# Optimization experiments

Measured on AMD Instinct MI355X. Metric: run time of the kernel, lower is better.

Reference implementation:

```python
import jax, jax.numpy as jnp
import numpy as np

ALPHA = 0.5
SPLIT_RATIO = 0.5
NUM_HEADS = 12
LN_EPS = 1e-6


def _layernorm(x, g, b):
    m = x.mean(-1, keepdims=True)
    v = ((x - m) ** 2).mean(-1, keepdims=True)
    return (x - m) * jax.lax.rsqrt(v + LN_EPS) * g + b


def setup_inputs() -> dict:
    key = jax.random.key(0)
    ks = jax.random.split(key, 8)
    B, N1, C, L, Hm = 16, 197, 768, 4, 3072
    s = 0.02
    return {
        "x": jax.random.normal(ks[0], (B, N1, C), jnp.float32),
        "glb_cls_attn": jax.random.uniform(ks[1], (B, N1 - 1), jnp.float32),
        "split_w": jax.random.normal(ks[2], (C, 4 * C), jnp.float32) * s,
        "split_b": jnp.zeros((4 * C,), jnp.float32),
        "ln1_g": jnp.ones((L, C), jnp.float32),
        "ln1_b": jnp.zeros((L, C), jnp.float32),
        "qkv_w": jax.random.normal(ks[3], (L, C, 3 * C), jnp.float32) * s,
        "qkv_b": jnp.zeros((L, 3 * C), jnp.float32),
        "proj_w": jax.random.normal(ks[4], (L, C, C), jnp.float32) * s,
        "proj_b": jnp.zeros((L, C), jnp.float32),
        "ln2_g": jnp.ones((L, C), jnp.float32),
        "ln2_b": jnp.zeros((L, C), jnp.float32),
        "fc1_w": jax.random.normal(ks[5], (L, C, Hm), jnp.float32) * s,
        "fc1_b": jnp.zeros((L, Hm), jnp.float32),
        "fc2_w": jax.random.normal(ks[6], (L, Hm, C), jnp.float32) * s,
        "fc2_b": jnp.zeros((L, C), jnp.float32),
    }


def reference(x, glb_cls_attn, split_w, split_b, ln1_g, ln1_b, qkv_w, qkv_b,
              proj_w, proj_b, ln2_g, ln2_b, fc1_w, fc1_b, fc2_w, fc2_b):
    B, _, C = x.shape
    H = NUM_HEADS
    D = C // H
    scale = D ** -0.5

    # --- token split based on global cls attention importance ---
    cls_tok, tokens = x[:, :1], x[:, 1:]
    order = jnp.argsort(-glb_cls_attn, axis=1)  # descending importance
    tokens = jnp.take_along_axis(tokens, order[:, :, None], axis=1)
    n = tokens.shape[1]
    split_n = int(n * SPLIT_RATIO)
    st = tokens[:, :split_n] @ split_w + split_b          # [B, split_n, 4C]
    st = st.reshape(B, split_n * 4, C)                    # each token -> 4 tokens
    x = jnp.concatenate([cls_tok, st, tokens[:, split_n:]], axis=1)
    N = x.shape[1]
    glb = jnp.zeros((B, N - 1), x.dtype)

    def block(carry, p):
        x, g = carry
        g1, b1, qw, qb, pw, pb, g2, b2, w1, bb1, w2, bb2 = p
        h = _layernorm(x, g1, b1)
        qkv = (h @ qw + qb).reshape(B, N, 3, H, D).transpose(2, 0, 3, 1, 4)
        q, k, v = qkv[0], qkv[1], qkv[2]                  # [B,H,N,D]
        attn = jax.nn.softmax(jnp.einsum('bhnd,bhmd->bhnm', q, k) * scale, axis=-1)
        cls_attn = attn[:, :, 0, 1:].mean(axis=1)         # mean over heads, row 0
        o = jnp.einsum('bhnm,bhmd->bhnd', attn, v).transpose(0, 2, 1, 3).reshape(B, N, C)
        x = x + o @ pw + pb
        h2 = _layernorm(x, g2, b2)
        x = x + jax.nn.gelu(h2 @ w1 + bb1, approximate=False) @ w2 + bb2
        g = ALPHA * g + (1.0 - ALPHA) * cls_attn
        return (x, g), None

    (x, glb), _ = jax.lax.scan(
        block, (x, glb),
        (ln1_g, ln1_b, qkv_w, qkv_b, proj_w, proj_b,
         ln2_g, ln2_b, fc1_w, fc1_b, fc2_w, fc2_b))
    return x, glb
```

## Files before the change

### kernel.cpp

```cpp
#include <hip/hip_runtime.h>
#include <math.h>

typedef unsigned short u16;
typedef short s16x8 __attribute__((ext_vector_type(8)));
typedef float f32x4 __attribute__((ext_vector_type(4)));

#define BB 16
#define N1 197
#define NTOK 196
#define SPLITN 98
#define NN 491
#define CC 768
#define H3 2304
#define HM 3072
#define NH 12
#define NL 4
#define BN (BB*NN)
#define MSPLIT (BB*SPLITN)

__device__ __forceinline__ float b2f(u16 u) {
    union { unsigned int i; float f; } x; x.i = ((unsigned int)u) << 16; return x.f;
}
__device__ __forceinline__ u16 f2b(float f) {
    union { float f; unsigned int i; } x; x.f = f;
    unsigned int i = x.i;
    return (u16)((i + 0x7fffu + ((i >> 16) & 1u)) >> 16);
}
__device__ __forceinline__ float ldx(const void* p, long long i, int isf32) {
    return isf32 ? ((const float*)p)[i] : b2f(((const u16*)p)[i]);
}

__device__ __forceinline__ void gload_lds16(const u16* g, u16* l) {
    __builtin_amdgcn_global_load_lds(
        (const __attribute__((address_space(1))) unsigned int*)g,
        (__attribute__((address_space(3))) unsigned int*)l,
        16, 0, 0);
}

__global__ void detect_k(const void* __restrict__ ln1_g, int* __restrict__ flag) {
    unsigned int w = ((const unsigned int*)ln1_g)[0];
    *flag = (w == 0x3F800000u) ? 1 : 0;
}

__global__ void zero_out_k(u16* __restrict__ out, long long n) {
    long long idx = (long long)blockIdx.x * 256 + threadIdx.x;
    if (idx < n) out[idx] = 0;
}

__global__ void zero_glb_k(float* __restrict__ glb) {
    int idx = blockIdx.x * 256 + threadIdx.x;
    if (idx < BB * (NN - 1)) glb[idx] = 0.0f;
}

__global__ void sort_k(const void* __restrict__ g, int* __restrict__ order,
                       const int* __restrict__ dflag) {
    __shared__ float v[256];
    int isf32 = *dflag;
    int b = blockIdx.x, t = threadIdx.x;
    float vv = -1e30f;
    if (t < NTOK) {
        vv = ldx(g, (long long)b * NTOK + t, isf32);
        if (!(vv == vv)) vv = -1e30f;
    }
    v[t] = vv;
    __syncthreads();
    if (t < NTOK) {
        float mv = v[t]; int r = 0;
        for (int j = 0; j < NTOK; j++) {
            float vj = v[j];
            if (vj > mv || (vj == mv && j < t)) r++;
        }
        order[b * NTOK + r] = t;
    }
}

__device__ __forceinline__ int clamp_tok(int tok) {
    return (tok < 0) ? 0 : (tok > NTOK - 1 ? NTOK - 1 : tok);
}

__global__ void gather_split_k(const void* __restrict__ x_in, const int* __restrict__ order,
                               u16* __restrict__ Asp, const int* __restrict__ dflag) {
    int isf32 = *dflag;
    long long idx = (long long)blockIdx.x * 256 + threadIdx.x;
    if (idx >= (long long)MSPLIT * CC) return;
    int c = (int)(idx % CC); int m = (int)(idx / CC); int b = m / SPLITN, r = m % SPLITN;
    int tok = clamp_tok(order[b * NTOK + r]);
    Asp[idx] = f2b(ldx(x_in, ((long long)b * N1 + 1 + tok) * CC + c, isf32));
}

__global__ void build_x_k(const void* __restrict__ x_in, const u16* __restrict__ st,
                          const int* __restrict__ order, float* __restrict__ x,
                          const int* __restrict__ dflag) {
    int isf32 = *dflag;
    long long idx = (long long)blockIdx.x * 256 + threadIdx.x;
    if (idx >= (long long)BN * CC) return;
    int c = (int)(idx % CC);
    int m = (int)(idx / CC);
    int b = m / NN, pos = m % NN;
    float v;
    if (pos == 0) {
        v = ldx(x_in, (long long)b * N1 * CC + c, isf32);
    } else if (pos < 1 + 4 * SPLITN) {
        int tt = pos - 1; int r = tt >> 2, kq = tt & 3;
        v = b2f(st[((long long)b * SPLITN + r) * HM + kq * CC + c]);
    } else {
        int j = pos - (1 + 4 * SPLITN);
        int tok = clamp_tok(order[b * NTOK + SPLITN + j]);
        v = ldx(x_in, ((long long)b * N1 + 1 + tok) * CC + c, isf32);
    }
    x[idx] = v;
}

__global__ void transpose_off_k(const void* __restrict__ in, u16* __restrict__ out, int K, int N,
                                long long off, const int* __restrict__ dflag) {
    __shared__ u16 tile[32][33];
    int isf32 = *dflag;
    int n0 = blockIdx.x * 32, k0 = blockIdx.y * 32;
    int tx = threadIdx.x, ty = threadIdx.y;
    for (int i = ty; i < 32; i += 8)
        tile[i][tx] = f2b(ldx(in, off + (long long)(k0 + i) * N + n0 + tx, isf32));
    __syncthreads();
    for (int i = ty; i < 32; i += 8) out[(long long)(n0 + i) * K + k0 + tx] = tile[tx][i];
}

__global__ __launch_bounds__(256) void ln_k(const float* __restrict__ x, const void* __restrict__ g,
                                            const void* __restrict__ bgain, u16* __restrict__ h,
                                            int goff, const int* __restrict__ dflag) {
    __shared__ float sb[8];
    int isf32 = *dflag;
    int row = blockIdx.x, t = threadIdx.x;
    const float* xr = x + (long long)row * CC;
    float v0 = xr[t], v1 = xr[t + 256], v2 = xr[t + 512];
    float s = v0 + v1 + v2;
    for (int o = 32; o > 0; o >>= 1) s += __shfl_down(s, o, 64);
    int lane = t & 63, w = t >> 6;
    if (lane == 0) sb[w] = s;
    __syncthreads();
    float mean = (sb[0] + sb[1] + sb[2] + sb[3]) * (1.0f / 768.0f);
    float d0 = v0 - mean, d1 = v1 - mean, d2 = v2 - mean;
    float q = d0 * d0 + d1 * d1 + d2 * d2;
    for (int o = 32; o > 0; o >>= 1) q += __shfl_down(q, o, 64);
    if (lane == 0) sb[4 + w] = q;
    __syncthreads();
    float var = (sb[4] + sb[5] + sb[6] + sb[7]) * (1.0f / 768.0f);
    float rs = rsqrtf(var + 1e-6f);
    long long o0 = (long long)row * CC;
    h[o0 + t]       = f2b(d0 * rs * ldx(g, goff + t, isf32)       + ldx(bgain, goff + t, isf32));
    h[o0 + t + 256] = f2b(d1 * rs * ldx(g, goff + t + 256, isf32) + ldx(bgain, goff + t + 256, isf32));
    h[o0 + t + 512] = f2b(d2 * rs * ldx(g, goff + t + 512, isf32) + ldx(bgain, goff + t + 512, isf32));
}

template<int TBM, int TBN>
__global__ __launch_bounds__(256) void gemm_t(const u16* __restrict__ A, const u16* __restrict__ BT,
                                              const void* __restrict__ bias, int boff,
                                              void* __restrict__ out,
                                              int M, int N, int K, int mode,
                                              const int* __restrict__ dflag) {
    constexpr int WM = TBM / 2, WN = TBN / 2, FM = WM / 16, FN = WN / 16;
    constexpr int AI = TBM / 64;
    constexpr int BI = TBN / 64;
    __shared__ __align__(16) u16 As[2][TBM * 32];
    __shared__ __align__(16) u16 Bs[2][TBN * 32];
    int isf32 = *dflag;

    int gx = gridDim.x, gy = gridDim.y;
    int nwg = gx * gy;
    int bid0 = blockIdx.y * gx + blockIdx.x;
    int q = nwg >> 3, rr = nwg & 7;
    int xcd = bid0 & 7, sl = bid0 >> 3;
    int wg = (xcd < rr ? xcd * (q + 1) : rr * (q + 1) + (xcd - rr) * q) + sl;
    int by = wg % gy, bx = wg / gy;
    int m0 = bx * TBM, n0 = by * TBN;

    int t = threadIdx.x, wave = t >> 6, lane = t & 63;
    int wm = (wave >> 1) * WM, wn = (wave & 1) * WN;
    int fr = lane & 15, quad = lane >> 4;

    int srow = lane >> 2;
    int scol = ((lane & 3) ^ ((srow >> 1) & 3)) * 8;

    f32x4 acc[FM][FN];
#pragma unroll
    for (int i = 0; i < FM; i++)
#pragma unroll
        for (int j = 0; j < FN; j++) acc[i][j] = (f32x4){0.f, 0.f, 0.f, 0.f};

    const int nk = K >> 5;

    auto stage = [&](int buf, int k0) {
#pragma unroll
        for (int i = 0; i < AI; i++) {
            int r0 = wave * (TBM / 4) + i * 16;
            int row = m0 + r0 + srow;
            if (row > M - 1) row = M - 1;
            gload_lds16(&A[(long long)row * K + k0 + scol], &As[buf][r0 * 32]);
        }
#pragma unroll
        for (int i = 0; i < BI; i++) {
            int r0 = wave * (TBN / 4) + i * 16;
            gload_lds16(&BT[(long long)(n0 + r0 + srow) * K + k0 + scol], &Bs[buf][r0 * 32]);
        }
    };

    stage(0, 0);
    __syncthreads();
    int rofs = ((quad ^ ((fr >> 1) & 3)) * 8);
    for (int kt = 0; kt < nk; kt++) {
        int cur = kt & 1;
        if (kt + 1 < nk) stage(cur ^ 1, (kt + 1) << 5);
        s16x8 af[FM], bf2[FN];
#pragma unroll
        for (int i = 0; i < FM; i++)
            af[i] = *(const s16x8*)&As[cur][(wm + i * 16 + fr) * 32 + rofs];
#pragma unroll
        for (int j = 0; j < FN; j++)
            bf2[j] = *(const s16x8*)&Bs[cur][(wn + j * 16 + fr) * 32 + rofs];
#pragma unroll
        for (int i = 0; i < FM; i++)
#pragma unroll
            for (int j = 0; j < FN; j++)
                acc[i][j] = __builtin_amdgcn_mfma_f32_16x16x32_bf16(af[i], bf2[j], acc[i][j], 0, 0, 0);
        __syncthreads();
    }

#pragma unroll
    for (int i = 0; i < FM; i++) {
#pragma unroll
        for (int j = 0; j < FN; j++) {
#pragma unroll
            for (int r = 0; r < 4; r++) {
                int row = m0 + wm + i * 16 + quad * 4 + r;
                int col = n0 + wn + j * 16 + fr;
                if (row < M) {
                    float v = acc[i][j][r] + ldx(bias, boff + col, isf32);
                    long long idx = (long long)row * N + col;
                    if (mode == 1) ((u16*)out)[idx] = f2b(v);
                    else if (mode == 2) {
                        float gl = 0.5f * v * (1.0f + erff(v * 0.70710678118654752f));
                        ((u16*)out)[idx] = f2b(gl);
                    } else ((float*)out)[idx] += v;
                }
            }
        }
    }
}

__global__ __launch_bounds__(256, 2) void attn_mfma_k(const u16* __restrict__ qkv,
                                                      u16* __restrict__ o,
                                                      float* __restrict__ cls_partial, int b0) {
    int bh = blockIdx.y; int lb = bh / NH, h = bh % NH;
    int i0 = blockIdx.x * 64;
    int w = threadIdx.x >> 6, lane = threadIdx.x & 63;
    int fr = lane & 15, quad = lane >> 4;
    int fk = quad * 8;

    __shared__ __align__(16) u16 Qs[64][72];
    __shared__ __align__(16) u16 Ks[64][72];
    __shared__ __align__(16) u16 Vt[64][40];
    __shared__ __align__(16) u16 Pst[4][16][40];

    const long long rowbase = (long long)lb * NN * H3 + (long long)h * 64;

    {
        int t = threadIdx.x;
#pragma unroll
        for (int i = 0; i < 2; i++) {
            int e = t + i * 256;
            int r = e >> 3, c8 = (e & 7) * 8;
            uint4 v = make_uint4(0u, 0u, 0u, 0u);
            int qrow = i0 + r;
            if (qrow < NN) v = *(const uint4*)&qkv[rowbase + (long long)qrow * H3 + c8];
            *(uint4*)&Qs[r][c8] = v;
        }
    }
    __syncthreads();
    s16x8 aq0 = *(const s16x8*)&Qs[w * 16 + fr][fk];
    s16x8 aq1 = *(const s16x8*)&Qs[w * 16 + fr][32 + fk];

    f32x4 S[32];
#pragma unroll
    for (int i = 0; i < 32; i++) S[i] = (f32x4){0.f, 0.f, 0.f, 0.f};

#pragma unroll
    for (int kt = 0; kt < 8; kt++) {
        int tb = kt * 64;
        __syncthreads();
        {
            int t = threadIdx.x;
#pragma unroll
            for (int i = 0; i < 2; i++) {
                int e = t + i * 256;
                int r = e >> 3, c8 = (e & 7) * 8;
                uint4 v = make_uint4(0u, 0u, 0u, 0u);
                int krow = tb + r;
                if (krow < NN) v = *(const uint4*)&qkv[rowbase + (long long)krow * H3 + CC + c8];
                *(uint4*)&Ks[r][c8] = v;
            }
        }
        __syncthreads();
#pragma unroll
        for (int ct = 0; ct < 4; ct++) {
            s16x8 bk0 = *(const s16x8*)&Ks[ct * 16 + fr][fk];
            s16x8 bk1 = *(const s16x8*)&Ks[ct * 16 + fr][32 + fk];
            S[kt * 4 + ct] = __builtin_amdgcn_mfma_f32_16x16x32_bf16(aq0, bk0, S[kt * 4 + ct], 0, 0, 0);
            S[kt * 4 + ct] = __builtin_amdgcn_mfma_f32_16x16x32_bf16(aq1, bk1, S[kt * 4 + ct], 0, 0, 0);
        }
    }

    float mrow[4] = {-1e30f, -1e30f, -1e30f, -1e30f};
#pragma unroll
    for (int tl = 0; tl < 32; tl++) {
        int col = tl * 16 + fr;
        bool valid = col < NN;
#pragma unroll
        for (int r = 0; r < 4; r++) {
            float s = S[tl][r] * 0.125f;
            s = valid ? s : -1e30f;
            S[tl][r] = s;
            mrow[r] = fmaxf(mrow[r], s);
        }
    }
#pragma unroll
    for (int m = 1; m < 16; m <<= 1)
#pragma unroll
        for (int r = 0; r < 4; r++) mrow[r] = fmaxf(mrow[r], __shfl_xor(mrow[r], m, 64));
    float lrow[4] = {0.f, 0.f, 0.f, 0.f};
#pragma unroll
    for (int tl = 0; tl < 32; tl++)
#pragma unroll
        for (int r = 0; r < 4; r++) {
            float e = __expf(S[tl][r] - mrow[r]);
            S[tl][r] = e;
            lrow[r] += e;
        }
#pragma unroll
    for (int m = 1; m < 16; m <<= 1)
#pragma unroll
        for (int r = 0; r < 4; r++) lrow[r] += __shfl_xor(lrow[r], m, 64);
    float linv[4];
#pragma unroll
    for (int r = 0; r < 4; r++) linv[r] = 1.0f / lrow[r];

    if (blockIdx.x == 0 && w == 0 && quad == 0) {
        long long cbase = (long long)((b0 + lb) * NH + h) * (NN - 1);
        float inv = linv[0];
#pragma unroll
        for (int tl = 0; tl < 32; tl++) {
            int col = tl * 16 + fr;
            if (col >= 1 && col < NN) cls_partial[cbase + col - 1] = S[tl][0] * inv;
        }
    }

    f32x4 O[4];
#pragma unroll
    for (int d = 0; d < 4; d++) O[d] = (f32x4){0.f, 0.f, 0.f, 0.f};
#pragma unroll
    for (int kt2 = 0; kt2 < 16; kt2++) {
        int vb = kt2 * 32;
        __syncthreads();
        {
            int t = threadIdx.x;
            int r = t >> 3, c8 = (t & 7) * 8;
            uint4 v = make_uint4(0u, 0u, 0u, 0u);
            int vrow = vb + r;
            if (vrow < NN) v = *(const uint4*)&qkv[rowbase + (long long)vrow * H3 + 2 * CC + c8];
            union { uint4 u; u16 e[8]; } tmp; tmp.u = v;
#pragma unroll
            for (int j = 0; j < 8; j++) Vt[c8 + j][r] = tmp.e[j];
        }
#pragma unroll
        for (int tt = 0; tt < 2; tt++) {
            int tl = kt2 * 2 + tt;
#pragma unroll
            for (int r = 0; r < 4; r++)
                Pst[w][quad * 4 + r][tt * 16 + fr] = f2b(S[tl][r]);
        }
        __syncthreads();
        s16x8 ap = *(const s16x8*)&Pst[w][fr][fk];
#pragma unroll
        for (int dt = 0; dt < 4; dt++) {
            s16x8 bv = *(const s16x8*)&Vt[dt * 16 + fr][fk];
            O[dt] = __builtin_amdgcn_mfma_f32_16x16x32_bf16(ap, bv, O[dt], 0, 0, 0);
        }
    }

#pragma unroll
    for (int r = 0; r < 4; r++) {
        int qrow = i0 + w * 16 + quad * 4 + r;
        if (qrow < NN) {
            long long obase = ((long long)(b0 + lb) * NN + qrow) * CC + h * 64;
#pragma unroll
            for (int dt = 0; dt < 4; dt++)
                o[obase + dt * 16 + fr] = f2b(O[dt][r] * linv[r]);
        }
    }
}

__global__ void glb_update_k(const float* __restrict__ cls_partial, float* __restrict__ glb) {
    int idx = blockIdx.x * 256 + threadIdx.x;
    if (idx >= BB * (NN - 1)) return;
    int b = idx / (NN - 1), j = idx % (NN - 1);
    float s = 0;
    for (int h = 0; h < NH; h++) s += cls_partial[(long long)(b * NH + h) * (NN - 1) + j];
    glb[idx] = 0.5f * glb[idx] + 0.5f * (s / NH);
}

__global__ void finalize_k(const float* __restrict__ x, const float* __restrict__ glb,
                           void* __restrict__ out, const int* __restrict__ dflag) {
    int isf32 = *dflag;
    long long nx = (long long)BN * CC;
    long long nt = nx + (long long)BB * (NN - 1);
    long long idx = (long long)blockIdx.x * 256 + threadIdx.x;
    if (idx >= nt) return;
    float v = (idx < nx) ? x[idx] : glb[idx - nx];
    if (isf32) ((float*)out)[idx] = v;
    else ((u16*)out)[idx] = f2b(v);
}

static inline char* carve(char*& p, size_t bytes) {
    char* r = p;
    p += (bytes + 255) & ~(size_t)255;
    return r;
}
static inline size_t padb(size_t b) { return (b + 255) & ~(size_t)255; }

extern "C" void kernel_launch(void* const* d_in, const int* in_sizes, int n_in,
                              void* d_out, int out_size, void* d_ws, size_t ws_size,
                              hipStream_t stream) {
    const void* x_in    = d_in[0];
    const void* glb_in  = d_in[1];
    const void* split_w = d_in[2];
    const void* split_b = d_in[3];
    const void* ln1_g   = d_in[4];
    const void* ln1_b   = d_in[5];
    const void* qkv_w   = d_in[6];
    const void* qkv_b   = d_in[7];
    const void* proj_w  = d_in[8];
    const void* proj_b  = d_in[9];
    const void* ln2_g   = d_in[10];
    const void* ln2_b   = d_in[11];
    const void* fc1_w   = d_in[12];
    const void* fc1_b   = d_in[13];
    const void* fc2_w   = d_in[14];
    const void* fc2_b   = d_in[15];

    const size_t sz_x    = (size_t)BN * CC * 4;
    const size_t sz_h    = (size_t)BN * CC * 2;
    const size_t sz_wt   = (size_t)HM * CC * 2;
    const size_t sz_cls  = (size_t)BB * NH * (NN - 1) * 4;
    const size_t sz_glb  = (size_t)BB * (NN - 1) * 4;
    const size_t sz_ord  = (size_t)BB * NTOK * 4;

    const size_t rA = (size_t)BN * H3 * 2;
    const size_t rB = (size_t)(BN / 4) * HM * 2;
    const size_t rC = (size_t)MSPLIT * HM * 2;

    const size_t base = padb(sz_x) + padb(sz_h) + 2 * padb(sz_wt) + padb(sz_cls) +
                        padb(sz_glb) + padb(sz_ord) + 256;
    int tier; size_t rsz;
    if (ws_size >= base + padb(rA))      { tier = 0; rsz = rA; }
    else if (ws_size >= base + padb(rB)) { tier = 1; rsz = rB; }
    else if (ws_size >= base + padb(rC)) { tier = 2; rsz = rC; }
    else {
        zero_out_k<<<(int)(((long long)out_size + 255) / 256), 256, 0, stream>>>((u16*)d_out, (long long)out_size);
        return;
    }

    char* p = (char*)d_ws;
    float* x_f32   = (float*)carve(p, sz_x);
    u16* h_buf     = (u16*)carve(p, sz_h);
    u16* region1   = (u16*)carve(p, rsz);
    u16* wtA       = (u16*)carve(p, sz_wt);
    u16* wtB       = (u16*)carve(p, sz_wt);
    float* cls_par = (float*)carve(p, sz_cls);
    float* glb_f32 = (float*)carve(p, sz_glb);
    int* order     = (int*)carve(p, sz_ord);
    int* dflag     = (int*)carve(p, 256);
    u16* Asp       = wtB;

    auto gemm = [&](const u16* A, const u16* BT, const void* bias, int boff, void* out,
                    int M, int N, int K, int mode) {
        long long b128 = (long long)((M + 127) / 128) * (N / 128);
        if ((N & 127) == 0 && b128 >= 512)
            gemm_t<128, 128><<<dim3((M + 127) / 128, N / 128), 256, 0, stream>>>(
                A, BT, bias, boff, out, M, N, K, mode, dflag);
        else
            gemm_t<64, 64><<<dim3((M + 63) / 64, N / 64), 256, 0, stream>>>(
                A, BT, bias, boff, out, M, N, K, mode, dflag);
    };

    dim3 tb(32, 8);
    detect_k<<<1, 1, 0, stream>>>(ln1_g, dflag);
    zero_glb_k<<<(BB * (NN - 1) + 255) / 256, 256, 0, stream>>>(glb_f32);
    sort_k<<<BB, 256, 0, stream>>>(glb_in, order, dflag);
    gather_split_k<<<(MSPLIT * CC + 255) / 256, 256, 0, stream>>>(x_in, order, Asp, dflag);
    transpose_off_k<<<dim3(HM / 32, CC / 32), tb, 0, stream>>>(split_w, wtA, CC, HM, 0, dflag);
    gemm(Asp, wtA, split_b, 0, region1, MSPLIT, HM, CC, 1);
    build_x_k<<<(int)(((long long)BN * CC + 255) / 256), 256, 0, stream>>>(x_in, region1, order,
                                                                           x_f32, dflag);

    const int QTILES = (NN + 63) / 64;
    const int bch  = (tier == 0) ? BB : 4;
    const int nbch = BB / bch;
    const int matt = bch * NN;
    const int nmch = (tier == 0) ? 2 : (tier == 1) ? 4 : 8;
    const int mch  = BN / nmch;

    for (int l = 0; l < NL; l++) {
        transpose_off_k<<<dim3(H3 / 32, CC / 32), tb, 0, stream>>>(qkv_w, wtA, CC, H3,
                                                                   (long long)l * CC * H3, dflag);
        ln_k<<<BN, 256, 0, stream>>>(x_f32, ln1_g, ln1_b, h_buf, l * CC, dflag);
        for (int bc = 0; bc < nbch; bc++) {
            const u16* Ain = h_buf + (long long)bc * matt * CC;
            gemm(Ain, wtA, qkv_b, l * H3, region1, matt, H3, CC, 1);
            attn_mfma_k<<<dim3(QTILES, bch * NH), 256, 0, stream>>>(region1, h_buf, cls_par, bc * bch);
        }
        glb_update_k<<<(BB * (NN - 1) + 255) / 256, 256, 0, stream>>>(cls_par, glb_f32);
        transpose_off_k<<<dim3(CC / 32, CC / 32), tb, 0, stream>>>(proj_w, wtA, CC, CC,
                                                                   (long long)l * CC * CC, dflag);
        gemm(h_buf, wtA, proj_b, l * CC, x_f32, BN, CC, CC, 3);
        ln_k<<<BN, 256, 0, stream>>>(x_f32, ln2_g, ln2_b, h_buf, l * CC, dflag);
        transpose_off_k<<<dim3(HM / 32, CC / 32), tb, 0, stream>>>(fc1_w, wtA, CC, HM,
                                                                   (long long)l * CC * HM, dflag);
        transpose_off_k<<<dim3(CC / 32, HM / 32), tb, 0, stream>>>(fc2_w, wtB, HM, CC,
                                                                   (long long)l * HM * CC, dflag);
        for (int mc = 0; mc < nmch; mc++) {
            const u16* Ain = h_buf + (long long)mc * mch * CC;
            float* xout    = x_f32 + (long long)mc * mch * CC;
            gemm(Ain, wtA, fc1_b, l * HM, region1, mch, HM, CC, 2);
            gemm(region1, wtB, fc2_b, l * CC, xout, mch, CC, HM, 3);
        }
    }
    long long total_out = (long long)BN * CC + (long long)BB * (NN - 1);
    finalize_k<<<(int)((total_out + 255) / 256), 256, 0, stream>>>(x_f32, glb_f32, d_out, dflag);
}
```

Baseline: 1.879 ms.

## Remap attention grid for XCD locality, widen PV tiles, swizzle V transpose

The attention kernel now launches a 1D grid and decodes block ids so that all 8 query tiles of a (batch, head) pair land on the same XCD, aiming for better L2 reuse of K/V. The PV loop processes 64 keys per step instead of 32, halving the barriers and doing two MFMAs per step. The transposed V tile is stored with an XOR swizzle to reduce LDS bank conflicts on both the scatter writes and the MFMA operand reads. The cost is more shared memory per block, and the id mapping assumes nbh is a multiple of 8 and exactly 8 query tiles.

```diff
diff --git a/kernel.cpp b/kernel.cpp
--- a/kernel.cpp
+++ b/kernel.cpp
@@ -247,17 +247,23 @@
 
 __global__ __launch_bounds__(256, 2) void attn_mfma_k(const u16* __restrict__ qkv,
                                                       u16* __restrict__ o,
-                                                      float* __restrict__ cls_partial, int b0) {
-    int bh = blockIdx.y; int lb = bh / NH, h = bh % NH;
-    int i0 = blockIdx.x * 64;
+                                                      float* __restrict__ cls_partial, int b0,
+                                                      int nbh) {
+    int bid = blockIdx.x;
+    int chunk = nbh >> 3;
+    int xcd = bid & 7, s = bid >> 3;
+    int qt = s & 7;
+    int bh = xcd * chunk + (s >> 3);
+    int lb = bh / NH, h = bh % NH;
+    int i0 = qt * 64;
     int w = threadIdx.x >> 6, lane = threadIdx.x & 63;
     int fr = lane & 15, quad = lane >> 4;
     int fk = quad * 8;
 
     __shared__ __align__(16) u16 Qs[64][72];
     __shared__ __align__(16) u16 Ks[64][72];
-    __shared__ __align__(16) u16 Vt[64][40];
-    __shared__ __align__(16) u16 Pst[4][16][40];
+    __shared__ __align__(16) u16 Vt[64][72];
+    __shared__ __align__(16) u16 Pst[4][16][72];
 
     const long long rowbase = (long long)lb * NN * H3 + (long long)h * 64;
 
@@ -314,10 +320,10 @@
         bool valid = col < NN;
 #pragma unroll
         for (int r = 0; r < 4; r++) {
-            float s = S[tl][r] * 0.125f;
-            s = valid ? s : -1e30f;
-            S[tl][r] = s;
-            mrow[r] = fmaxf(mrow[r], s);
+            float s2 = S[tl][r] * 0.125f;
+            s2 = valid ? s2 : -1e30f;
+            S[tl][r] = s2;
+            mrow[r] = fmaxf(mrow[r], s2);
         }
     }
 #pragma unroll
@@ -341,7 +347,7 @@
 #pragma unroll
     for (int r = 0; r < 4; r++) linv[r] = 1.0f / lrow[r];
 
-    if (blockIdx.x == 0 && w == 0 && quad == 0) {
+    if (qt == 0 && w == 0 && quad == 0) {
         long long cbase = (long long)((b0 + lb) * NH + h) * (NN - 1);
         float inv = linv[0];
 #pragma unroll
@@ -355,32 +361,46 @@
 #pragma unroll
     for (int d = 0; d < 4; d++) O[d] = (f32x4){0.f, 0.f, 0.f, 0.f};
 #pragma unroll
-    for (int kt2 = 0; kt2 < 16; kt2++) {
-        int vb = kt2 * 32;
+    for (int kt2 = 0; kt2 < 8; kt2++) {
+        int vb = kt2 * 64;
         __syncthreads();
         {
             int t = threadIdx.x;
-            int r = t >> 3, c8 = (t & 7) * 8;
-            uint4 v = make_uint4(0u, 0u, 0u, 0u);
-            int vrow = vb + r;
-            if (vrow < NN) v = *(const uint4*)&qkv[rowbase + (long long)vrow * H3 + 2 * CC + c8];
-            union { uint4 u; u16 e[8]; } tmp; tmp.u = v;
-#pragma unroll
-            for (int j = 0; j < 8; j++) Vt[c8 + j][r] = tmp.e[j];
-        }
-#pragma unroll
-        for (int tt = 0; tt < 2; tt++) {
-            int tl = kt2 * 2 + tt;
+#pragma unroll
+            for (int i = 0; i < 2; i++) {
+                int e = t + i * 256;
+                int r = e >> 3, c8 = (e & 7) * 8;
+                uint4 v = make_uint4(0u, 0u, 0u, 0u);
+                int vrow = vb + r;
+                if (vrow < NN) v = *(const uint4*)&qkv[rowbase + (long long)vrow * H3 + 2 * CC + c8];
+                union { uint4 u; u16 e8[8]; } tmp; tmp.u = v;
+                int rblk = r >> 3, rin = r & 7;
+#pragma unroll
+                for (int j = 0; j < 8; j++) {
+                    int row = c8 + j;
+                    int cp = ((rblk ^ (row >> 3)) << 3) | rin;
+                    Vt[row][cp] = tmp.e8[j];
+                }
+            }
+        }
+#pragma unroll
+        for (int tt = 0; tt < 4; tt++) {
+            int tl = kt2 * 4 + tt;
 #pragma unroll
             for (int r = 0; r < 4; r++)
                 Pst[w][quad * 4 + r][tt * 16 + fr] = f2b(S[tl][r]);
         }
         __syncthreads();
-        s16x8 ap = *(const s16x8*)&Pst[w][fr][fk];
+        s16x8 ap0 = *(const s16x8*)&Pst[w][fr][fk];
+        s16x8 ap1 = *(const s16x8*)&Pst[w][fr][32 + fk];
 #pragma unroll
         for (int dt = 0; dt < 4; dt++) {
-            s16x8 bv = *(const s16x8*)&Vt[dt * 16 + fr][fk];
-            O[dt] = __builtin_amdgcn_mfma_f32_16x16x32_bf16(ap, bv, O[dt], 0, 0, 0);
+            int row = dt * 16 + fr;
+            int g = row >> 3;
+            s16x8 bv0 = *(const s16x8*)&Vt[row][((quad ^ g) & 7) * 8];
+            s16x8 bv1 = *(const s16x8*)&Vt[row][(((4 + quad) ^ g) & 7) * 8];
+            O[dt] = __builtin_amdgcn_mfma_f32_16x16x32_bf16(ap0, bv0, O[dt], 0, 0, 0);
+            O[dt] = __builtin_amdgcn_mfma_f32_16x16x32_bf16(ap1, bv1, O[dt], 0, 0, 0);
         }
     }
 
@@ -499,10 +519,10 @@
     build_x_k<<<(int)(((long long)BN * CC + 255) / 256), 256, 0, stream>>>(x_in, region1, order,
                                                                            x_f32, dflag);
 
-    const int QTILES = (NN + 63) / 64;
     const int bch  = (tier == 0) ? BB : 4;
     const int nbch = BB / bch;
     const int matt = bch * NN;
+    const int nbh  = bch * NH;
     const int nmch = (tier == 0) ? 2 : (tier == 1) ? 4 : 8;
     const int mch  = BN / nmch;
 
@@ -513,7 +533,7 @@
         for (int bc = 0; bc < nbch; bc++) {
             const u16* Ain = h_buf + (long long)bc * matt * CC;
             gemm(Ain, wtA, qkv_b, l * H3, region1, matt, H3, CC, 1);
-            attn_mfma_k<<<dim3(QTILES, bch * NH), 256, 0, stream>>>(region1, h_buf, cls_par, bc * bch);
+            attn_mfma_k<<<dim3(nbh * 8), 256, 0, stream>>>(region1, h_buf, cls_par, bc * bch, nbh);
         }
         glb_update_k<<<(BB * (NN - 1) + 255) / 256, 256, 0, stream>>>(cls_par, glb_f32);
         transpose_off_k<<<dim3(CC / 32, CC / 32), tb, 0, stream>>>(proj_w, wtA, CC, CC,
```

New measurement: 1.788 ms. 1.05x faster.
